# Performance work log

Hardware: AMD Instinct MI355X
Metric: run time of the kernel (lower is better)

Reference implementation:

```python
import jax, jax.numpy as jnp
import numpy as np

N_MIX = 2


def setup_inputs() -> dict:
    key = jax.random.key(0)
    k1, k2, k3, k4 = jax.random.split(key, 4)
    B, d_k, N = 8, 512, 2048
    qt = jax.random.normal(k1, (B, d_k, N), dtype=jnp.float32)
    kt = jax.random.normal(k2, (B, d_k, N), dtype=jnp.float32)
    vt = jax.random.normal(k3, (B, d_k, N), dtype=jnp.float32)
    std = N_MIX ** -0.5
    weight = jax.random.uniform(k4, (N_MIX, d_k), dtype=jnp.float32, minval=-std, maxval=std)
    return {"qt": qt, "kt": kt, "vt": vt, "weight": weight}


def reference(qt, kt, vt, weight):
    # qt: [B, d_k, N], kt: [B, d_k, N2], vt: [B, d_v, N2], weight: [m, d_k]
    B, d_k, N = qt.shape
    N2 = kt.shape[2]
    m = N_MIX
    d = d_k // m
    temperature = jnp.float32(d_k ** 0.5)  # note: sqrt(d_k), not sqrt(d)

    # mixture weights pi: softmax over the m mixture components
    bar_qt = jnp.mean(qt, axis=2)  # [B, d_k]
    pi = jax.nn.softmax(jnp.einsum('md,bd->bm', weight, bar_qt), axis=1)  # [B, m]
    pi = pi.reshape(B * m, 1, 1)

    q = jnp.transpose(qt.reshape(B * m, d, N), (0, 2, 1))  # [B*m, N, d]
    k = kt.reshape(B * m, d, N2)                            # [B*m, d, N2]
    v = jnp.transpose(vt, (0, 2, 1))                        # [B, N2, d_v]

    attn = jnp.matmul(q, k) / temperature                   # [B*m, N, N2]
    attn = jax.nn.softmax(attn, axis=2)
    # dropout is identity at inference
    attn = (attn * pi).reshape(B, m, N, N2).sum(axis=1)     # [B, N, N2]

    output = jnp.matmul(attn, v)                            # [B, N, d_v]
    return output, attn
```

## Files before the change

### kernel.cpp

```cpp
#include <hip/hip_runtime.h>
#include <stdint.h>

typedef unsigned short u16;
typedef float f32x4 __attribute__((ext_vector_type(4)));
typedef _Float16 half8 __attribute__((ext_vector_type(8)));
typedef __fp16 fp16x2 __attribute__((ext_vector_type(2)));

#define B_  8
#define M_  2
#define DK_ 512
#define D_  256
#define N_  2048
#define DV_ 512

#define OUT_FLOATS (B_*N_*DV_)
#define QB_U16     (B_*M_*N_*D_)

__device__ __forceinline__ uint32_t pk16(float a, float b){
    fp16x2 h = __builtin_amdgcn_cvt_pkrtz(a, b);
    return __builtin_bit_cast(uint32_t, h);
}
__device__ __forceinline__ float h2f_lo(uint32_t u){
    return (float)__builtin_bit_cast(_Float16, (unsigned short)(u & 0xffffu));
}
__device__ __forceinline__ float h2f_hi(uint32_t u){
    return (float)__builtin_bit_cast(_Float16, (unsigned short)(u >> 16));
}

__global__ __launch_bounds__(256) void k0_transpose(const float* __restrict__ qt,
                                                    const float* __restrict__ kt,
                                                    u16* __restrict__ dstBase){
    const int it = blockIdx.x, yc = blockIdx.y, z = blockIdx.z;
    const int b = z & 7, src = z >> 3;
    const float* sp = src ? kt : qt;
    u16* dp = dstBase + (size_t)src * QB_U16;
    const int m = yc >> 2;
    const int cbase = (yc & 3) * 64;
    const int i0 = it * 64;
    __shared__ u16 lds[64 * 72];
    const int t = threadIdx.x;
    {
        const int c_loc = t >> 2;
        const int iq = (t & 3) * 16;
        const float* g = sp + (size_t)(b*DK_ + m*D_ + cbase + c_loc) * N_ + i0 + iq;
        float vv[16];
        *(float4*)&vv[0]  = *(const float4*)(g + 0);
        *(float4*)&vv[4]  = *(const float4*)(g + 4);
        *(float4*)&vv[8]  = *(const float4*)(g + 8);
        *(float4*)&vv[12] = *(const float4*)(g + 12);
        #pragma unroll
        for (int e = 0; e < 16; ++e){
            _Float16 hf = (_Float16)vv[e];
            lds[(iq + e)*72 + c_loc] = __builtin_bit_cast(unsigned short, hf);
        }
    }
    __syncthreads();
    {
        const int i_loc = t >> 2;
        const int cq = (t & 3) * 16;
        uint4 a  = *(const uint4*)&lds[i_loc*72 + cq];
        uint4 b2 = *(const uint4*)&lds[i_loc*72 + cq + 8];
        u16* o = dp + (size_t)((b*M_ + m)*N_ + i0 + i_loc) * D_ + cbase + cq;
        *(uint4*)o = a;
        *(uint4*)(o + 8) = b2;
    }
}

__global__ __launch_bounds__(256) void k0_vconv(const float* __restrict__ vt,
                                                u16* __restrict__ vB){
    size_t idx = ((size_t)blockIdx.x * 256 + threadIdx.x) * 8;
    const size_t total = (size_t)B_ * DV_ * N_;
    if (idx < total){
        float4 f0 = *(const float4*)(vt + idx);
        float4 f1 = *(const float4*)(vt + idx + 4);
        uint4 o;
        o.x = pk16(f0.x, f0.y);
        o.y = pk16(f0.z, f0.w);
        o.z = pk16(f1.x, f1.y);
        o.w = pk16(f1.z, f1.w);
        *(uint4*)(vB + idx) = o;
    }
}

__global__ __launch_bounds__(256) void k1_bar(const float* __restrict__ qt,
                                              float* __restrict__ bar){
    const int cg = blockIdx.x, b = blockIdx.y;
    const int t = threadIdx.x;
    const int c = cg*8 + (t >> 5);
    const int seg = t & 31;
    const float* g = qt + (size_t)(b*DK_ + c)*N_ + seg*64;
    float s = 0.f;
    #pragma unroll
    for (int k = 0; k < 16; ++k){
        float4 f = *(const float4*)(g + k*4);
        s += f.x + f.y + f.z + f.w;
    }
    s += __shfl_xor(s, 1); s += __shfl_xor(s, 2); s += __shfl_xor(s, 4);
    s += __shfl_xor(s, 8); s += __shfl_xor(s, 16);
    if (seg == 0) bar[b*DK_ + c] = s * (1.f / (float)N_);
}

__global__ void k2_logits(const float* __restrict__ wgt,
                          const float* __restrict__ bar,
                          float* __restrict__ wsLog){
    const int bm = blockIdx.x;
    const int b = bm >> 1, m = bm & 1;
    const int l = threadIdx.x;
    float s = 0.f;
    #pragma unroll
    for (int k = 0; k < 8; ++k){
        const int c = l + k*64;
        s += wgt[m*DK_ + c] * bar[b*DK_ + c];
    }
    s += __shfl_xor(s, 1); s += __shfl_xor(s, 2); s += __shfl_xor(s, 4);
    s += __shfl_xor(s, 8); s += __shfl_xor(s, 16); s += __shfl_xor(s, 32);
    if (l == 0) wsLog[bm] = s;
}

__global__ __launch_bounds__(256, 2) void k3_qk(const u16* __restrict__ qB,
                                                const u16* __restrict__ kB,
                                                uint32_t* __restrict__ attnE){
    const int jt = blockIdx.x, it = blockIdx.y, b = blockIdx.z;
    const int t = threadIdx.x;
    const int w = t >> 6, l = t & 63;
    const int wi = w & 1, wj = w >> 1;
    const int l15 = l & 15, lq = l >> 4;
    __shared__ u16 lds[4 * 128 * 64];

    f32x4 acc[2][4][4] = {};

    const int srow = t >> 1, shalf = t & 1;
    for (int bk = 0; bk < 4; ++bk){
        #pragma unroll
        for (int tile = 0; tile < 4; ++tile){
            const int qk = tile >> 1, m = tile & 1;
            const u16* sp = qk ? kB : qB;
            const int row0 = (qk ? jt : it) * 128;
            const u16* g = sp + (size_t)((b*M_ + m)*N_ + row0 + srow) * D_ + bk*64 + shalf*32;
            const uint4* gp = (const uint4*)g;
            uint4 v0 = gp[0], v1 = gp[1], v2 = gp[2], v3 = gp[3];
            u16* base = &lds[(tile*128 + srow) * 64];
            const int rs = srow & 7;
            *(uint4*)&base[((shalf*4 + 0) ^ rs) * 8] = v0;
            *(uint4*)&base[((shalf*4 + 1) ^ rs) * 8] = v1;
            *(uint4*)&base[((shalf*4 + 2) ^ rs) * 8] = v2;
            *(uint4*)&base[((shalf*4 + 3) ^ rs) * 8] = v3;
        }
        __syncthreads();
        #pragma unroll
        for (int ks = 0; ks < 2; ++ks){
            #pragma unroll
            for (int m = 0; m < 2; ++m){
                half8 a[4], bb[4];
                #pragma unroll
                for (int ti = 0; ti < 4; ++ti){
                    const int row = wi*64 + ti*16 + l15;
                    const int gr = (ks*4 + lq) ^ (row & 7);
                    a[ti] = *(const half8*)&lds[(m*128 + row)*64 + gr*8];
                }
                #pragma unroll
                for (int tj = 0; tj < 4; ++tj){
                    const int row = wj*64 + tj*16 + l15;
                    const int gr = (ks*4 + lq) ^ (row & 7);
                    bb[tj] = *(const half8*)&lds[((2 + m)*128 + row)*64 + gr*8];
                }
                #pragma unroll
                for (int ti = 0; ti < 4; ++ti)
                    #pragma unroll
                    for (int tj = 0; tj < 4; ++tj)
                        acc[m][ti][tj] = __builtin_amdgcn_mfma_f32_16x16x32_f16(
                            a[ti], bb[tj], acc[m][ti][tj], 0, 0, 0);
            }
        }
        __syncthreads();
    }

    const float INVT = 0.04419417382415922f;
    uint32_t* op = attnE + (size_t)b * N_ * N_;
    const int ibase = it*128 + wi*64;
    const int jbase = jt*128 + wj*64;
    #pragma unroll
    for (int ti = 0; ti < 4; ++ti){
        #pragma unroll
        for (int tj = 0; tj < 4; ++tj){
            #pragma unroll
            for (int rr = 0; rr < 4; ++rr){
                const int i = ibase + ti*16 + lq*4 + rr;
                const int j = jbase + tj*16 + l15;
                const float e0 = __expf(acc[0][ti][tj][rr] * INVT);
                const float e1 = __expf(acc[1][ti][tj][rr] * INVT);
                op[(size_t)i * N_ + j] = pk16(e0, e1);
            }
        }
    }
}

__global__ __launch_bounds__(256) void k35_rowsum(const uint32_t* __restrict__ attnE,
                                                  const float* __restrict__ wsLog,
                                                  float* __restrict__ wsScale){
    const int blk = blockIdx.x;
    const int b = blk >> 9;
    const int w = threadIdx.x >> 6, l = threadIdx.x & 63;
    const int i = (blk & 511)*4 + w;
    const uint4* e = (const uint4*)(attnE + ((size_t)b*N_ + i)*N_);
    float s0 = 0.f, s1 = 0.f;
    #pragma unroll
    for (int k = 0; k < 8; ++k){
        uint4 u = e[k*64 + l];
        s0 += h2f_lo(u.x) + h2f_lo(u.y) + h2f_lo(u.z) + h2f_lo(u.w);
        s1 += h2f_hi(u.x) + h2f_hi(u.y) + h2f_hi(u.z) + h2f_hi(u.w);
    }
    s0 += __shfl_xor(s0, 1);  s1 += __shfl_xor(s1, 1);
    s0 += __shfl_xor(s0, 2);  s1 += __shfl_xor(s1, 2);
    s0 += __shfl_xor(s0, 4);  s1 += __shfl_xor(s1, 4);
    s0 += __shfl_xor(s0, 8);  s1 += __shfl_xor(s1, 8);
    s0 += __shfl_xor(s0, 16); s1 += __shfl_xor(s1, 16);
    s0 += __shfl_xor(s0, 32); s1 += __shfl_xor(s1, 32);
    if (l == 0){
        const float lg0 = wsLog[b*2 + 0], lg1 = wsLog[b*2 + 1];
        const float pi0 = 1.f / (1.f + __expf(lg1 - lg0));
        const float pi1 = 1.f / (1.f + __expf(lg0 - lg1));
        wsScale[((size_t)b*N_ + i)*2 + 0] = pi0 / s0;
        wsScale[((size_t)b*N_ + i)*2 + 1] = pi1 / s1;
    }
}

template<bool HASVB>
__global__ __launch_bounds__(512) void k4_pv(const float* __restrict__ vt,
                                             const u16* __restrict__ vB,
                                             const float* __restrict__ wsScale,
                                             uint32_t* __restrict__ attnE,
                                             float* __restrict__ outO){
    const int itile = blockIdx.x, b = blockIdx.y;
    const int i0 = itile * 64;
    const int t = threadIdx.x;
    const int l = t & 63, w = t >> 6;
    const int l15 = l & 15, lq = l >> 4;
    const int rowgrp = w & 3, dvh = w >> 2;
    __shared__ u16 v_lds[2][16384];

    const int rl = rowgrp*16 + l15;
    const float2 p01 = *(const float2*)&wsScale[((size_t)(b*N_ + i0 + rl))*2];
    const float p0 = p01.x, p1 = p01.y;
    uint32_t* erow = attnE + (size_t)(b*N_ + i0 + rl) * N_;

    const u16*   gv16 = vB + (size_t)(b*DV_ + t)*N_;
    const float* gv32 = vt + (size_t)(b*DV_ + t)*N_;

    uint4  rv[4];
    float4 rf[8];

    auto issue_load = [&](int c){
        const int j0 = c*32;
        if (HASVB){
            const uint4* gp = (const uint4*)(gv16 + j0);
            rv[0] = gp[0]; rv[1] = gp[1]; rv[2] = gp[2]; rv[3] = gp[3];
        } else {
            const float4* gp = (const float4*)(gv32 + j0);
            #pragma unroll
            for (int q = 0; q < 8; ++q) rf[q] = gp[q];
        }
    };
    auto write_lds = [&](int buf){
        #pragma unroll
        for (int G = 0; G < 4; ++G){
            uint4 u;
            if (HASVB){
                u = rv[G];
            } else {
                u.x = pk16(rf[2*G].x,   rf[2*G].y);
                u.y = pk16(rf[2*G].z,   rf[2*G].w);
                u.z = pk16(rf[2*G+1].x, rf[2*G+1].y);
                u.w = pk16(rf[2*G+1].z, rf[2*G+1].w);
            }
            *(uint4*)&v_lds[buf][G*4096 + t*8] = u;
        }
    };

    f32x4 acc[16] = {};

    issue_load(0);
    write_lds(0);
    issue_load(1);
    uint4 e0 = *(const uint4*)(erow + lq*8);
    uint4 e1 = *(const uint4*)(erow + lq*8 + 4);
    __syncthreads();

    int cur = 0;
    for (int c = 0; c < 64; ++c){
        if (c + 1 < 64) write_lds(cur ^ 1);
        if (c + 2 < 64) issue_load(c + 2);
        uint4 en0, en1;
        if (c + 1 < 64){
            en0 = *(const uint4*)(erow + (c+1)*32 + lq*8);
            en1 = *(const uint4*)(erow + (c+1)*32 + lq*8 + 4);
        }
        float av[8];
        av[0] = p0*h2f_lo(e0.x) + p1*h2f_hi(e0.x);
        av[1] = p0*h2f_lo(e0.y) + p1*h2f_hi(e0.y);
        av[2] = p0*h2f_lo(e0.z) + p1*h2f_hi(e0.z);
        av[3] = p0*h2f_lo(e0.w) + p1*h2f_hi(e0.w);
        av[4] = p0*h2f_lo(e1.x) + p1*h2f_hi(e1.x);
        av[5] = p0*h2f_lo(e1.y) + p1*h2f_hi(e1.y);
        av[6] = p0*h2f_lo(e1.z) + p1*h2f_hi(e1.z);
        av[7] = p0*h2f_lo(e1.w) + p1*h2f_hi(e1.w);
        uint4 ua;
        ua.x = pk16(av[0], av[1]);
        ua.y = pk16(av[2], av[3]);
        ua.z = pk16(av[4], av[5]);
        ua.w = pk16(av[6], av[7]);
        union { uint4 u; half8 h; } cvt;
        cvt.u = ua;
        half8 af = cvt.h;

        __syncthreads();

        if (dvh == 0){
            uint32_t* ep = erow + c*32 + lq*8;
            float4 w0 = make_float4(av[0], av[1], av[2], av[3]);
            float4 w1 = make_float4(av[4], av[5], av[6], av[7]);
            *(float4*)ep = w0;
            *(float4*)(ep + 4) = w1;
        }

        const u16* vb = &v_lds[cur][lq*4096 + (dvh*256 + l15)*8];
        #pragma unroll
        for (int n = 0; n < 16; ++n){
            half8 bv = *(const half8*)(vb + n*128);
            acc[n] = __builtin_amdgcn_mfma_f32_16x16x32_f16(af, bv, acc[n], 0, 0, 0);
        }
        if (c + 1 < 64){ e0 = en0; e1 = en1; }
        __syncthreads();
        cur ^= 1;
    }

    #pragma unroll
    for (int n = 0; n < 16; ++n){
        #pragma unroll
        for (int rr = 0; rr < 4; ++rr){
            const int i  = i0 + rowgrp*16 + lq*4 + rr;
            const int dv = dvh*256 + n*16 + l15;
            outO[(size_t)(b*N_ + i)*DV_ + dv] = acc[n][rr];
        }
    }
}

extern "C" void kernel_launch(void* const* d_in, const int* in_sizes, int n_in,
                              void* d_out, int out_size, void* d_ws, size_t ws_size,
                              hipStream_t stream){
    const float* qt  = (const float*)d_in[0];
    const float* kt  = (const float*)d_in[1];
    const float* vt  = (const float*)d_in[2];
    const float* wgt = (const float*)d_in[3];

    float* ws      = (float*)d_ws;
    float* wsLog   = ws;
    float* wsBar   = ws + 16;
    float* wsScale = (float*)((char*)d_ws + 32768);

    u16* stage = (u16*)d_out;
    u16* kB = stage + QB_U16;
    uint32_t* attnE = (uint32_t*)d_out + OUT_FLOATS;
    float* outO = (float*)d_out;

    const size_t vbBytes = (size_t)B_ * DV_ * N_ * 2;
    u16* vB = (ws_size >= (size_t)262144 + vbBytes)
                  ? (u16*)((char*)d_ws + 262144) : (u16*)nullptr;

    k0_transpose<<<dim3(32, 8, 16), 256, 0, stream>>>(qt, kt, stage);
    if (vB) k0_vconv<<<dim3(4096), 256, 0, stream>>>(vt, vB);
    k1_bar<<<dim3(64, 8), 256, 0, stream>>>(qt, wsBar);
    k2_logits<<<dim3(16), 64, 0, stream>>>(wgt, wsBar, wsLog);
    k3_qk<<<dim3(16, 16, 8), 256, 0, stream>>>(stage, kB, attnE);
    k35_rowsum<<<dim3(4096), 256, 0, stream>>>(attnE, wsLog, wsScale);
    if (vB) k4_pv<true ><<<dim3(32, 8), 512, 0, stream>>>(vt, vB, wsScale, attnE, outO);
    else    k4_pv<false><<<dim3(32, 8), 512, 0, stream>>>(vt, vB, wsScale, attnE, outO);
}
```

Before: 239.3 us.

## Halve PV row tile, remove mid-loop barrier, defer attention writeback

```diff
diff --git a/kernel.cpp b/kernel.cpp
--- a/kernel.cpp
+++ b/kernel.cpp
@@ -232,14 +232,14 @@
                                              uint32_t* __restrict__ attnE,
                                              float* __restrict__ outO){
     const int itile = blockIdx.x, b = blockIdx.y;
-    const int i0 = itile * 64;
+    const int i0 = itile * 32;
     const int t = threadIdx.x;
     const int l = t & 63, w = t >> 6;
     const int l15 = l & 15, lq = l >> 4;
-    const int rowgrp = w & 3, dvh = w >> 2;
+    const int rg = w & 1, dvq = w >> 1;
     __shared__ u16 v_lds[2][16384];
 
-    const int rl = rowgrp*16 + l15;
+    const int rl = rg*16 + l15;
     const float2 p01 = *(const float2*)&wsScale[((size_t)(b*N_ + i0 + rl))*2];
     const float p0 = p01.x, p1 = p01.y;
     uint32_t* erow = attnE + (size_t)(b*N_ + i0 + rl) * N_;
@@ -247,10 +247,11 @@
     const u16*   gv16 = vB + (size_t)(b*DV_ + t)*N_;
     const float* gv32 = vt + (size_t)(b*DV_ + t)*N_;
 
-    uint4  rv[4];
-    float4 rf[8];
-
-    auto issue_load = [&](int c){
+    uint4  rvA[4], rvB[4];
+    float4 rfA[8], rfB[8];
+    uint4  e0A, e1A, e0B, e1B;
+
+    auto loadV = [&](uint4 (&rv)[4], float4 (&rf)[8], int c){
         const int j0 = c*32;
         if (HASVB){
             const uint4* gp = (const uint4*)(gv16 + j0);
@@ -261,7 +262,7 @@
             for (int q = 0; q < 8; ++q) rf[q] = gp[q];
         }
     };
-    auto write_lds = [&](int buf){
+    auto writeV = [&](int buf, uint4 (&rv)[4], float4 (&rf)[8]){
         #pragma unroll
         for (int G = 0; G < 4; ++G){
             uint4 u;
@@ -276,34 +277,41 @@
             *(uint4*)&v_lds[buf][G*4096 + t*8] = u;
         }
     };
-
-    f32x4 acc[16] = {};
-
-    issue_load(0);
-    write_lds(0);
-    issue_load(1);
-    uint4 e0 = *(const uint4*)(erow + lq*8);
-    uint4 e1 = *(const uint4*)(erow + lq*8 + 4);
+    auto loadE = [&](uint4& e0, uint4& e1, int c){
+        const uint4* p = (const uint4*)(erow + c*32 + lq*8);
+        e0 = p[0];
+        e1 = p[1];
+    };
+
+    f32x4 acc[8] = {};
+    float avP[8];
+
+    loadV(rvA, rfA, 0);
+    writeV(0, rvA, rfA);
+    loadV(rvB, rfB, 1);
+    loadE(e0A, e1A, 0);
     __syncthreads();
 
-    int cur = 0;
-    for (int c = 0; c < 64; ++c){
-        if (c + 1 < 64) write_lds(cur ^ 1);
-        if (c + 2 < 64) issue_load(c + 2);
-        uint4 en0, en1;
-        if (c + 1 < 64){
-            en0 = *(const uint4*)(erow + (c+1)*32 + lq*8);
-            en1 = *(const uint4*)(erow + (c+1)*32 + lq*8 + 4);
-        }
+    auto body = [&](int c, uint4 (&rvW)[4], float4 (&rfW)[8],
+                    uint4 (&rvL)[4], float4 (&rfL)[8],
+                    uint4& ec0, uint4& ec1, uint4& en0, uint4& en1){
+        if (c >= 1 && dvq == 0){
+            float* ap = (float*)(erow + (c-1)*32 + lq*8);
+            *(float4*)ap       = make_float4(avP[0], avP[1], avP[2], avP[3]);
+            *(float4*)(ap + 4) = make_float4(avP[4], avP[5], avP[6], avP[7]);
+        }
+        if (c + 1 < 64) loadE(en0, en1, c + 1);
+        if (c + 2 < 64) loadV(rvL, rfL, c + 2);
+
         float av[8];
-        av[0] = p0*h2f_lo(e0.x) + p1*h2f_hi(e0.x);
-        av[1] = p0*h2f_lo(e0.y) + p1*h2f_hi(e0.y);
-        av[2] = p0*h2f_lo(e0.z) + p1*h2f_hi(e0.z);
-        av[3] = p0*h2f_lo(e0.w) + p1*h2f_hi(e0.w);
-        av[4] = p0*h2f_lo(e1.x) + p1*h2f_hi(e1.x);
-        av[5] = p0*h2f_lo(e1.y) + p1*h2f_hi(e1.y);
-        av[6] = p0*h2f_lo(e1.z) + p1*h2f_hi(e1.z);
-        av[7] = p0*h2f_lo(e1.w) + p1*h2f_hi(e1.w);
+        av[0] = p0*h2f_lo(ec0.x) + p1*h2f_hi(ec0.x);
+        av[1] = p0*h2f_lo(ec0.y) + p1*h2f_hi(ec0.y);
+        av[2] = p0*h2f_lo(ec0.z) + p1*h2f_hi(ec0.z);
+        av[3] = p0*h2f_lo(ec0.w) + p1*h2f_hi(ec0.w);
+        av[4] = p0*h2f_lo(ec1.x) + p1*h2f_hi(ec1.x);
+        av[5] = p0*h2f_lo(ec1.y) + p1*h2f_hi(ec1.y);
+        av[6] = p0*h2f_lo(ec1.z) + p1*h2f_hi(ec1.z);
+        av[7] = p0*h2f_lo(ec1.w) + p1*h2f_hi(ec1.w);
         uint4 ua;
         ua.x = pk16(av[0], av[1]);
         ua.y = pk16(av[2], av[3]);
@@ -313,33 +321,34 @@
         cvt.u = ua;
         half8 af = cvt.h;
 
-        __syncthreads();
-
-        if (dvh == 0){
-            uint32_t* ep = erow + c*32 + lq*8;
-            float4 w0 = make_float4(av[0], av[1], av[2], av[3]);
-            float4 w1 = make_float4(av[4], av[5], av[6], av[7]);
-            *(float4*)ep = w0;
-            *(float4*)(ep + 4) = w1;
-        }
-
-        const u16* vb = &v_lds[cur][lq*4096 + (dvh*256 + l15)*8];
-        #pragma unroll
-        for (int n = 0; n < 16; ++n){
+        const u16* vb = &v_lds[c & 1][lq*4096 + (dvq*128 + l15)*8];
+        #pragma unroll
+        for (int n = 0; n < 8; ++n){
             half8 bv = *(const half8*)(vb + n*128);
             acc[n] = __builtin_amdgcn_mfma_f32_16x16x32_f16(af, bv, acc[n], 0, 0, 0);
         }
-        if (c + 1 < 64){ e0 = en0; e1 = en1; }
+        if (c + 1 < 64) writeV((c + 1) & 1, rvW, rfW);
+        #pragma unroll
+        for (int q = 0; q < 8; ++q) avP[q] = av[q];
         __syncthreads();
-        cur ^= 1;
-    }
-
-    #pragma unroll
-    for (int n = 0; n < 16; ++n){
+    };
+
+    for (int c = 0; c < 64; c += 2){
+        body(c,     rvB, rfB, rvA, rfA, e0A, e1A, e0B, e1B);
+        body(c + 1, rvA, rfA, rvB, rfB, e0B, e1B, e0A, e1A);
+    }
+    if (dvq == 0){
+        float* ap = (float*)(erow + 63*32 + lq*8);
+        *(float4*)ap       = make_float4(avP[0], avP[1], avP[2], avP[3]);
+        *(float4*)(ap + 4) = make_float4(avP[4], avP[5], avP[6], avP[7]);
+    }
+
+    #pragma unroll
+    for (int n = 0; n < 8; ++n){
         #pragma unroll
         for (int rr = 0; rr < 4; ++rr){
-            const int i  = i0 + rowgrp*16 + lq*4 + rr;
-            const int dv = dvh*256 + n*16 + l15;
+            const int i  = i0 + rg*16 + lq*4 + rr;
+            const int dv = dvq*128 + n*16 + l15;
             outO[(size_t)(b*N_ + i)*DV_ + dv] = acc[n][rr];
         }
     }
@@ -373,6 +382,6 @@
     k2_logits<<<dim3(16), 64, 0, stream>>>(wgt, wsBar, wsLog);
     k3_qk<<<dim3(16, 16, 8), 256, 0, stream>>>(stage, kB, attnE);
     k35_rowsum<<<dim3(4096), 256, 0, stream>>>(attnE, wsLog, wsScale);
-    if (vB) k4_pv<true ><<<dim3(32, 8), 512, 0, stream>>>(vt, vB, wsScale, attnE, outO);
-    else    k4_pv<false><<<dim3(32, 8), 512, 0, stream>>>(vt, vB, wsScale, attnE, outO);
-}
+    if (vB) k4_pv<true ><<<dim3(64, 8), 512, 0, stream>>>(vt, vB, wsScale, attnE, outO);
+    else    k4_pv<false><<<dim3(64, 8), 512, 0, stream>>>(vt, vB, wsScale, attnE, outO);
+}
```

Result: slower. 329.5 us (+37.7%).
